# Kernel tuning notes

Hardware: AMD Instinct MI355X
Metric: run time of the kernel (lower is better)

Reference implementation:

```python
import jax, jax.numpy as jnp
from jax import lax
import numpy as np

K = 31      # avg_pool2d kernel_size
PAD = 15    # avg_pool2d padding
EPS = 1.0
GAMMA = 5.0


def _box_avg(x):
    # Separable 31x31 box filter, stride 1, zero padding 15,
    # count_include_pad=True (PyTorch default) -> always divide by K*K.
    s = lax.reduce_window(x, 0.0, lax.add, (1, 1, K, 1), (1, 1, 1, 1),
                          [(0, 0), (0, 0), (PAD, PAD), (0, 0)])
    s = lax.reduce_window(s, 0.0, lax.add, (1, 1, 1, K), (1, 1, 1, 1),
                          [(0, 0), (0, 0), (0, 0), (PAD, PAD)])
    return s / (K * K)


def setup_inputs() -> dict:
    key = jax.random.key(0)
    k1, k2 = jax.random.split(key)
    shape = (64, 1, 512, 512)  # [B, C, H, W]
    inp = jax.random.uniform(k1, shape, dtype=jnp.float32)
    tgt = jax.random.uniform(k2, shape, dtype=jnp.float32)
    return {"input": inp, "target": tgt}


def reference(input, target):
    weight = 1.0 + GAMMA * jnp.abs(_box_avg(target) - target)
    intersection = jnp.sum(input * target * weight)
    denom = jnp.sum(input * weight) + jnp.sum(target * weight)
    dice = (2.0 * intersection + EPS) / (denom + EPS)
    return 1.0 - dice
```

## Files before the change

### kernel.cpp

```cpp
#include <hip/hip_runtime.h>


#define BATCH 64
#define H     512
#define W     512
#define KW    31
#define PADR  15

#define NSEG  32
#define SEG   (H / NSEG)

#define HBOX_BLOCKS (BATCH * H / 4)

__global__ __launch_bounds__(256) void vbox_kernel(const float* __restrict__ tgt,
                                                   float* __restrict__ colsum) {
    const int t    = blockIdx.x * 256 + threadIdx.x;
    const int w4   = t & (W / 4 - 1);
    const int rest = t >> 7;
    const int seg  = rest & (NSEG - 1);
    const int b    = rest >> 5;
    const size_t base = (size_t)b * H * W + (size_t)w4 * 4;
    const int h0 = seg * SEG;

    float rx = 0.f, ry = 0.f, rz = 0.f, rw = 0.f;
    #pragma unroll
    for (int j = -PADR; j <= PADR; ++j) {
        const int r = h0 + j;
        if (r >= 0 && r < H) {
            const float4 v = *(const float4*)(tgt + base + (size_t)r * W);
            rx += v.x; ry += v.y; rz += v.z; rw += v.w;
        }
    }

    #pragma unroll
    for (int h = h0; h < h0 + SEG; ++h) {
        float4 o; o.x = rx; o.y = ry; o.z = rz; o.w = rw;
        *(float4*)(colsum + base + (size_t)h * W) = o;
        const int add = h + PADR + 1;
        const int sub = h - PADR;
        if (add < H) {
            const float4 v = *(const float4*)(tgt + base + (size_t)add * W);
            rx += v.x; ry += v.y; rz += v.z; rw += v.w;
        }
        if (sub >= 0) {
            const float4 v = *(const float4*)(tgt + base + (size_t)sub * W);
            rx -= v.x; ry -= v.y; rz -= v.z; rw -= v.w;
        }
    }
}

__global__ __launch_bounds__(256) void hbox_reduce_kernel(const float* __restrict__ colsum,
                                                          const float* __restrict__ tgt,
                                                          const float* __restrict__ inp,
                                                          float4* __restrict__ partials) {
    const int wave = threadIdx.x >> 6;
    const int lane = threadIdx.x & 63;
    const int row  = blockIdx.x * 4 + wave;
    const size_t rowbase = (size_t)row * W;
    const int col0 = lane * 8;

    float r[40];
    const float* p = colsum + rowbase + col0 - 16;
    #pragma unroll
    for (int k = 0; k < 10; ++k) {
        const float4 v = *(const float4*)(p + 4 * k);
        r[4 * k + 0] = v.x; r[4 * k + 1] = v.y;
        r[4 * k + 2] = v.z; r[4 * k + 3] = v.w;
    }
    #pragma unroll
    for (int k = 0; k < 40; ++k) {
        const int c = col0 - 16 + k;
        if (c < 0 || c >= W) r[k] = 0.f;
    }

    float run = 0.f;
    #pragma unroll
    for (int k = 1; k <= 31; ++k) run += r[k];

    const float4 t0 = *(const float4*)(tgt + rowbase + col0);
    const float4 t1 = *(const float4*)(tgt + rowbase + col0 + 4);
    const float4 i0 = *(const float4*)(inp + rowbase + col0);
    const float4 i1 = *(const float4*)(inp + rowbase + col0 + 4);
    const float tv[8] = {t0.x, t0.y, t0.z, t0.w, t1.x, t1.y, t1.z, t1.w};
    const float iv[8] = {i0.x, i0.y, i0.z, i0.w, i1.x, i1.y, i1.z, i1.w};

    const float inv = 1.0f / (float)(KW * KW);
    float aI = 0.f, aA = 0.f, aB = 0.f;
    #pragma unroll
    for (int j = 0; j < 8; ++j) {
        const float wgt = 1.0f + 5.0f * fabsf(run * inv - tv[j]);
        aI += iv[j] * tv[j] * wgt;
        aA += iv[j] * wgt;
        aB += tv[j] * wgt;
        run += r[j + 32] - r[j + 1];
    }

    #pragma unroll
    for (int off = 32; off > 0; off >>= 1) {
        aI += __shfl_down(aI, off, 64);
        aA += __shfl_down(aA, off, 64);
        aB += __shfl_down(aB, off, 64);
    }

    __shared__ float part[3][4];
    if (lane == 0) {
        part[0][wave] = aI; part[1][wave] = aA; part[2][wave] = aB;
    }
    __syncthreads();
    if (threadIdx.x == 0) {
        float4 o;
        o.x = part[0][0] + part[0][1] + part[0][2] + part[0][3];
        o.y = part[1][0] + part[1][1] + part[1][2] + part[1][3];
        o.z = part[2][0] + part[2][1] + part[2][2] + part[2][3];
        o.w = 0.f;
        partials[blockIdx.x] = o;
    }
}

__global__ __launch_bounds__(1024) void reduce_kernel(const float4* __restrict__ partials,
                                                      float* __restrict__ out) {
    const int tid = threadIdx.x;
    float aI = 0.f, aA = 0.f, aB = 0.f;
    #pragma unroll
    for (int i = tid; i < HBOX_BLOCKS; i += 1024) {
        const float4 v = partials[i];
        aI += v.x; aA += v.y; aB += v.z;
    }
    #pragma unroll
    for (int off = 32; off > 0; off >>= 1) {
        aI += __shfl_down(aI, off, 64);
        aA += __shfl_down(aA, off, 64);
        aB += __shfl_down(aB, off, 64);
    }
    __shared__ float s[3][16];
    const int wv = tid >> 6, ln = tid & 63;
    if (ln == 0) { s[0][wv] = aI; s[1][wv] = aA; s[2][wv] = aB; }
    __syncthreads();
    if (tid == 0) {
        float I = 0.f, A = 0.f, Bv = 0.f;
        #pragma unroll
        for (int k = 0; k < 16; ++k) { I += s[0][k]; A += s[1][k]; Bv += s[2][k]; }
        out[0] = 1.0f - (2.0f * I + 1.0f) / (A + Bv + 1.0f);
    }
}

extern "C" void kernel_launch(void* const* d_in, const int* in_sizes, int n_in,
                              void* d_out, int out_size, void* d_ws, size_t ws_size,
                              hipStream_t stream) {
    const float* inp = (const float*)d_in[0];
    const float* tgt = (const float*)d_in[1];
    float* out = (float*)d_out;

    float4* partials = (float4*)((char*)d_ws + 256);
    float*  colsum   = (float*)((char*)d_ws + 256 + (size_t)HBOX_BLOCKS * 16);

    vbox_kernel<<<BATCH * NSEG * (W / 4) / 256, 256, 0, stream>>>(tgt, colsum);
    hbox_reduce_kernel<<<HBOX_BLOCKS, 256, 0, stream>>>(colsum, tgt, inp, partials);
    reduce_kernel<<<1, 1024, 0, stream>>>(partials, out);
}
```

Before: 182.1 us.

## Fuse vertical and horizontal box passes into one wave-per-band kernel

Replaces the separate vertical column-sum kernel and the horizontal reduce kernel with a single kernel. One 64-lane wave keeps running column sums in registers for a 16-row band and builds the horizontal window with cross-lane shuffles. This removes the intermediate column-sum buffer write and read from global memory. In exchange, there are fewer, smaller blocks (one wave each), which lowers occupancy and makes each wave iterate serially over rows.

```diff
diff --git a/kernel.cpp b/kernel.cpp
--- a/kernel.cpp
+++ b/kernel.cpp
@@ -4,95 +4,94 @@
 #define BATCH 64
 #define H     512
 #define W     512
-#define KW    31
 #define PADR  15
+#define NSEG  32
+#define RB    (H / NSEG)
+#define NBLK  (BATCH * NSEG)
 
-#define NSEG  32
-#define SEG   (H / NSEG)
+__global__ __launch_bounds__(64) void fused_kernel(const float* __restrict__ tgt,
+                                                   const float* __restrict__ inp,
+                                                   float4* __restrict__ partials) {
+    const int lane = threadIdx.x;
+    const int blk  = blockIdx.x;
+    const int band = blk & (NSEG - 1);
+    const int b    = blk >> 5;
+    const int r0   = band * RB;
+    const int col0 = lane * 8;
+    const float* timg = tgt + (size_t)b * H * W;
+    const float* iimg = inp + (size_t)b * H * W;
 
-#define HBOX_BLOCKS (BATCH * H / 4)
-
-__global__ __launch_bounds__(256) void vbox_kernel(const float* __restrict__ tgt,
-                                                   float* __restrict__ colsum) {
-    const int t    = blockIdx.x * 256 + threadIdx.x;
-    const int w4   = t & (W / 4 - 1);
-    const int rest = t >> 7;
-    const int seg  = rest & (NSEG - 1);
-    const int b    = rest >> 5;
-    const size_t base = (size_t)b * H * W + (size_t)w4 * 4;
-    const int h0 = seg * SEG;
-
-    float rx = 0.f, ry = 0.f, rz = 0.f, rw = 0.f;
+    float vr[8];
+    #pragma unroll
+    for (int k = 0; k < 8; ++k) vr[k] = 0.f;
     #pragma unroll
     for (int j = -PADR; j <= PADR; ++j) {
-        const int r = h0 + j;
+        const int r = r0 + j;
         if (r >= 0 && r < H) {
-            const float4 v = *(const float4*)(tgt + base + (size_t)r * W);
-            rx += v.x; ry += v.y; rz += v.z; rw += v.w;
+            const float4 a = *(const float4*)(timg + (size_t)r * W + col0);
+            const float4 c = *(const float4*)(timg + (size_t)r * W + col0 + 4);
+            vr[0] += a.x; vr[1] += a.y; vr[2] += a.z; vr[3] += a.w;
+            vr[4] += c.x; vr[5] += c.y; vr[6] += c.z; vr[7] += c.w;
         }
     }
 
+    float validf[40];
     #pragma unroll
-    for (int h = h0; h < h0 + SEG; ++h) {
-        float4 o; o.x = rx; o.y = ry; o.z = rz; o.w = rw;
-        *(float4*)(colsum + base + (size_t)h * W) = o;
+    for (int m = 0; m < 40; ++m) {
+        const int c = col0 - 16 + m;
+        validf[m] = (c >= 0 && c < W) ? 1.f : 0.f;
+    }
+
+    const float inv = 1.0f / 961.0f;
+    float aI = 0.f, aA = 0.f, aB = 0.f;
+
+    for (int h = r0; h < r0 + RB; ++h) {
+        float wd[40];
+        #pragma unroll
+        for (int k = 0; k < 8; ++k) {
+            wd[k]      = __shfl_up(vr[k], 2, 64);
+            wd[k + 8]  = __shfl_up(vr[k], 1, 64);
+            wd[k + 16] = vr[k];
+            wd[k + 24] = __shfl_down(vr[k], 1, 64);
+            wd[k + 32] = __shfl_down(vr[k], 2, 64);
+        }
+        #pragma unroll
+        for (int m = 0; m < 40; ++m) wd[m] *= validf[m];
+
+        float run = 0.f;
+        #pragma unroll
+        for (int m = 1; m <= 31; ++m) run += wd[m];
+
+        const float4 t0 = *(const float4*)(timg + (size_t)h * W + col0);
+        const float4 t1 = *(const float4*)(timg + (size_t)h * W + col0 + 4);
+        const float4 i0 = *(const float4*)(iimg + (size_t)h * W + col0);
+        const float4 i1 = *(const float4*)(iimg + (size_t)h * W + col0 + 4);
+        const float tv[8] = {t0.x, t0.y, t0.z, t0.w, t1.x, t1.y, t1.z, t1.w};
+        const float iv[8] = {i0.x, i0.y, i0.z, i0.w, i1.x, i1.y, i1.z, i1.w};
+
+        #pragma unroll
+        for (int j = 0; j < 8; ++j) {
+            const float wgt = 1.0f + 5.0f * fabsf(run * inv - tv[j]);
+            aI += iv[j] * tv[j] * wgt;
+            aA += iv[j] * wgt;
+            aB += tv[j] * wgt;
+            run += wd[j + 32] - wd[j + 1];
+        }
+
         const int add = h + PADR + 1;
         const int sub = h - PADR;
         if (add < H) {
-            const float4 v = *(const float4*)(tgt + base + (size_t)add * W);
-            rx += v.x; ry += v.y; rz += v.z; rw += v.w;
+            const float4 a = *(const float4*)(timg + (size_t)add * W + col0);
+            const float4 c = *(const float4*)(timg + (size_t)add * W + col0 + 4);
+            vr[0] += a.x; vr[1] += a.y; vr[2] += a.z; vr[3] += a.w;
+            vr[4] += c.x; vr[5] += c.y; vr[6] += c.z; vr[7] += c.w;
         }
         if (sub >= 0) {
-            const float4 v = *(const float4*)(tgt + base + (size_t)sub * W);
-            rx -= v.x; ry -= v.y; rz -= v.z; rw -= v.w;
+            const float4 a = *(const float4*)(timg + (size_t)sub * W + col0);
+            const float4 c = *(const float4*)(timg + (size_t)sub * W + col0 + 4);
+            vr[0] -= a.x; vr[1] -= a.y; vr[2] -= a.z; vr[3] -= a.w;
+            vr[4] -= c.x; vr[5] -= c.y; vr[6] -= c.z; vr[7] -= c.w;
         }
-    }
-}
-
-__global__ __launch_bounds__(256) void hbox_reduce_kernel(const float* __restrict__ colsum,
-                                                          const float* __restrict__ tgt,
-                                                          const float* __restrict__ inp,
-                                                          float4* __restrict__ partials) {
-    const int wave = threadIdx.x >> 6;
-    const int lane = threadIdx.x & 63;
-    const int row  = blockIdx.x * 4 + wave;
-    const size_t rowbase = (size_t)row * W;
-    const int col0 = lane * 8;
-
-    float r[40];
-    const float* p = colsum + rowbase + col0 - 16;
-    #pragma unroll
-    for (int k = 0; k < 10; ++k) {
-        const float4 v = *(const float4*)(p + 4 * k);
-        r[4 * k + 0] = v.x; r[4 * k + 1] = v.y;
-        r[4 * k + 2] = v.z; r[4 * k + 3] = v.w;
-    }
-    #pragma unroll
-    for (int k = 0; k < 40; ++k) {
-        const int c = col0 - 16 + k;
-        if (c < 0 || c >= W) r[k] = 0.f;
-    }
-
-    float run = 0.f;
-    #pragma unroll
-    for (int k = 1; k <= 31; ++k) run += r[k];
-
-    const float4 t0 = *(const float4*)(tgt + rowbase + col0);
-    const float4 t1 = *(const float4*)(tgt + rowbase + col0 + 4);
-    const float4 i0 = *(const float4*)(inp + rowbase + col0);
-    const float4 i1 = *(const float4*)(inp + rowbase + col0 + 4);
-    const float tv[8] = {t0.x, t0.y, t0.z, t0.w, t1.x, t1.y, t1.z, t1.w};
-    const float iv[8] = {i0.x, i0.y, i0.z, i0.w, i1.x, i1.y, i1.z, i1.w};
-
-    const float inv = 1.0f / (float)(KW * KW);
-    float aI = 0.f, aA = 0.f, aB = 0.f;
-    #pragma unroll
-    for (int j = 0; j < 8; ++j) {
-        const float wgt = 1.0f + 5.0f * fabsf(run * inv - tv[j]);
-        aI += iv[j] * tv[j] * wgt;
-        aA += iv[j] * wgt;
-        aB += tv[j] * wgt;
-        run += r[j + 32] - r[j + 1];
     }
 
     #pragma unroll
@@ -101,19 +100,9 @@
         aA += __shfl_down(aA, off, 64);
         aB += __shfl_down(aB, off, 64);
     }
-
-    __shared__ float part[3][4];
     if (lane == 0) {
-        part[0][wave] = aI; part[1][wave] = aA; part[2][wave] = aB;
-    }
-    __syncthreads();
-    if (threadIdx.x == 0) {
-        float4 o;
-        o.x = part[0][0] + part[0][1] + part[0][2] + part[0][3];
-        o.y = part[1][0] + part[1][1] + part[1][2] + part[1][3];
-        o.z = part[2][0] + part[2][1] + part[2][2] + part[2][3];
-        o.w = 0.f;
-        partials[blockIdx.x] = o;
+        float4 o; o.x = aI; o.y = aA; o.z = aB; o.w = 0.f;
+        partials[blk] = o;
     }
 }
 
@@ -122,7 +111,7 @@
     const int tid = threadIdx.x;
     float aI = 0.f, aA = 0.f, aB = 0.f;
     #pragma unroll
-    for (int i = tid; i < HBOX_BLOCKS; i += 1024) {
+    for (int i = tid; i < NBLK; i += 1024) {
         const float4 v = partials[i];
         aI += v.x; aA += v.y; aB += v.z;
     }
@@ -151,10 +140,8 @@
     const float* tgt = (const float*)d_in[1];
     float* out = (float*)d_out;
 
-    float4* partials = (float4*)((char*)d_ws + 256);
-    float*  colsum   = (float*)((char*)d_ws + 256 + (size_t)HBOX_BLOCKS * 16);
+    float4* partials = (float4*)d_ws;
 
-    vbox_kernel<<<BATCH * NSEG * (W / 4) / 256, 256, 0, stream>>>(tgt, colsum);
-    hbox_reduce_kernel<<<HBOX_BLOCKS, 256, 0, stream>>>(colsum, tgt, inp, partials);
+    fused_kernel<<<NBLK, 64, 0, stream>>>(tgt, inp, partials);
     reduce_kernel<<<1, 1024, 0, stream>>>(partials, out);
 }
```

Measured after the change: 169.0 us. -7.2%, faster.
